# Optimization experiments

Measured on AMD Instinct MI355X. Metric: run time of the kernel, lower is better.

Reference implementation:

```python
import jax, jax.numpy as jnp
import numpy as np
from jax import lax

T, B, I, H = 32768, 1, 128, 512  # seq_len, batch(=1 due to squeeze(1)), input_dim, hidden_dim
HEAD = 25

def setup_inputs() -> dict:
    key = jax.random.key(0)
    ks = jax.random.split(key, 8)
    s = 1.0 / np.sqrt(H)  # pytorch LSTM init scale
    return {
        "x": jax.random.normal(ks[0], (T, B, I), dtype=jnp.float32),
        "W_ih": jax.random.uniform(ks[1], (4 * H, I), jnp.float32, -s, s),
        "W_hh": jax.random.uniform(ks[2], (4 * H, H), jnp.float32, -s, s),
        "b_ih": jax.random.uniform(ks[3], (4 * H,), jnp.float32, -s, s),
        "b_hh": jax.random.uniform(ks[4], (4 * H,), jnp.float32, -s, s),
        "W1": jax.random.uniform(ks[5], (HEAD, H), jnp.float32, -s, s),
        "b1": jax.random.uniform(ks[6], (HEAD,), jnp.float32, -s, s),
        "Wout": jax.random.uniform(ks[7], (1, HEAD), jnp.float32, -s, s),
    }

def reference(x, W_ih, W_hh, b_ih, b_hh, W1, b1, Wout):
    # Precompute input projections for all timesteps (one big GEMM): [T, B, 4H]
    xg = jnp.einsum('tbi,gi->tbg', x, W_ih) + (b_ih + b_hh)

    def step(carry, xg_t):
        h, c = carry  # [B, H] each
        gates = xg_t + h @ W_hh.T  # [B, 4H]
        i_g, f_g, g_g, o_g = jnp.split(gates, 4, axis=-1)  # pytorch gate order i,f,g,o
        i = jax.nn.sigmoid(i_g)
        f = jax.nn.sigmoid(f_g)
        g = jnp.tanh(g_g)
        o = jax.nn.sigmoid(o_g)
        c = f * c + i * g
        h = o * jnp.tanh(c)
        return (h, c), h

    h0 = jnp.zeros((B, H), x.dtype)
    _, hs = lax.scan(step, (h0, h0), xg)  # hs: [T, B, H]

    hid = hs[:, 0, :]  # h_1.squeeze(1) -> [T, H]
    # forward applies c1 then out (c2 is defined but unused in the original)
    out = (hid @ W1.T + b1) @ Wout.T  # [T, 1]
    return out
```

## Files before the change

kernel.cpp:

```cpp
#include <hip/hip_runtime.h>
#include <math.h>


#define T_SEQ 32768
#define HID   512
#define INP   128
#define NWG   32
#define NTH   512
#define HSL   16
#define KW    64
#define KX    16

typedef unsigned long long u64;

__device__ __forceinline__ float fast_sigmoid(float x) {
    return 1.0f / (1.0f + __expf(-x));
}
__device__ __forceinline__ float fast_tanh(float x) {
    float a = fabsf(x);
    float e = __expf(-2.0f * a);
    float r = (1.0f - e) / (1.0f + e);
    return copysignf(r, x);
}

__global__ void __launch_bounds__(NTH, 2) lstm_persist(
    const float* __restrict__ x,
    const float* __restrict__ W_ih,
    const float* __restrict__ W_hh,
    const float* __restrict__ b_ih,
    const float* __restrict__ b_hh,
    const float* __restrict__ W1,
    const float* __restrict__ Wout,
    u64* __restrict__ hbuf,
    float* __restrict__ out)
{
    const int w   = blockIdx.x;
    const int tid = threadIdx.x;
    const int rl  = tid >> 3;
    const int j   = tid & 7;
    const int grow = (rl >> 4) * HID + w * HSL + (rl & 15);

    __shared__ float h_lds[HID];
    __shared__ float gate_lds[64];

    float wr[KW];
#pragma unroll
    for (int kk = 0; kk < 16; ++kk) {
        const int p = (kk + 2 * j) & 15;
        const float4 wv = *(const float4*)&W_hh[grow * HID + j * KW + 4 * p];
        wr[4 * kk + 0] = wv.x; wr[4 * kk + 1] = wv.y;
        wr[4 * kk + 2] = wv.z; wr[4 * kk + 3] = wv.w;
    }
    float wi[KX];
#pragma unroll
    for (int k = 0; k < KX; k += 4) {
        const float4 wv = *(const float4*)&W_ih[grow * INP + j * KX + k];
        wi[k] = wv.x; wi[k + 1] = wv.y; wi[k + 2] = wv.z; wi[k + 3] = wv.w;
    }
    float brow = b_ih[grow] + b_hh[grow];
    float weff = 0.0f;
    if (tid < HSL) {
        const int col = w * HSL + tid;
        for (int p = 0; p < 25; ++p) weff += Wout[p] * W1[p * HID + col];
    }
#pragma unroll
    for (int k = 0; k < KW; ++k) asm volatile("" : "+v"(wr[k]));
#pragma unroll
    for (int k = 0; k < KX; ++k) asm volatile("" : "+v"(wi[k]));
    asm volatile("" : "+v"(brow));
    asm volatile("" : "+v"(weff));

    float c = 0.0f;
    float xa[KX];
#pragma unroll
    for (int k = 0; k < KX; ++k) xa[k] = x[j * KX + k];

    for (unsigned int t = 0; t < T_SEQ; ++t) {
        if (tid < 64) {
            const u64* P = hbuf + (t & 1) * HID;
            u64 pr[8];
            bool ok = false;
            do {
                if (!ok) {
                    ok = true;
#pragma unroll
                    for (int i = 0; i < 8; ++i) {
                        pr[i] = __hip_atomic_load(&P[tid + 64 * i],
                                                  __ATOMIC_RELAXED,
                                                  __HIP_MEMORY_SCOPE_AGENT);
                        ok = ok && ((unsigned int)(pr[i] >> 32) == t);
                    }
                }
            } while (__ballot(ok) != ~0ull);
#pragma unroll
            for (int i = 0; i < 8; ++i)
                h_lds[tid + 64 * i] = __uint_as_float((unsigned int)pr[i]);
        }
        __syncthreads();

        float a0 = 0.0f, a1 = 0.0f, a2 = 0.0f, a3 = 0.0f;
#pragma unroll
        for (int k = 0; k < KX; k += 4) {
            a0 += wi[k + 0] * xa[k + 0];
            a1 += wi[k + 1] * xa[k + 1];
            a2 += wi[k + 2] * xa[k + 2];
            a3 += wi[k + 3] * xa[k + 3];
        }
        const float4* hl4 = (const float4*)&h_lds[j * KW];
#pragma unroll
        for (int kk = 0; kk < 16; ++kk) {
            const int p = (kk + 2 * j) & 15;
            const float4 h4 = hl4[p];
            a0 += wr[4 * kk + 0] * h4.x;
            a1 += wr[4 * kk + 1] * h4.y;
            a2 += wr[4 * kk + 2] * h4.z;
            a3 += wr[4 * kk + 3] * h4.w;
        }
        const int tn = (t + 1 < T_SEQ) ? (int)(t + 1) : (int)t;
#pragma unroll
        for (int k = 0; k < KX; k += 4) {
            const float4 x4 = *(const float4*)&x[tn * INP + j * KX + k];
            xa[k + 0] = x4.x; xa[k + 1] = x4.y;
            xa[k + 2] = x4.z; xa[k + 3] = x4.w;
        }

        float acc = (a0 + a1) + (a2 + a3);
        acc += __shfl_xor(acc, 1);
        acc += __shfl_xor(acc, 2);
        acc += __shfl_xor(acc, 4);
        if (j == 0) gate_lds[rl] = acc + brow;
        __syncthreads();

        if (tid < HSL) {
            const float iv = fast_sigmoid(gate_lds[tid]);
            const float fv = fast_sigmoid(gate_lds[16 + tid]);
            const float gv = fast_tanh(gate_lds[32 + tid]);
            const float ov = fast_sigmoid(gate_lds[48 + tid]);
            c = fv * c + iv * gv;
            const float hv = ov * fast_tanh(c);
            const u64 pkt = ((u64)(t + 1) << 32) | (u64)__float_as_uint(hv);
            __hip_atomic_store(&hbuf[((t + 1) & 1) * HID + w * HSL + tid], pkt,
                               __ATOMIC_RELAXED, __HIP_MEMORY_SCOPE_AGENT);
            float pd = hv * weff;
            pd += __shfl_xor(pd, 1);
            pd += __shfl_xor(pd, 2);
            pd += __shfl_xor(pd, 4);
            pd += __shfl_xor(pd, 8);
            if (tid == 0) atomicAdd(&out[t], pd);
        }
    }
}

__global__ void init_out(const float* __restrict__ b1,
                         const float* __restrict__ Wout,
                         float* __restrict__ out)
{
    const int t = blockIdx.x * blockDim.x + threadIdx.x;
    float be = 0.0f;
    for (int p = 0; p < 25; ++p) be += b1[p] * Wout[p];
    if (t < T_SEQ) out[t] = be;
}

extern "C" void kernel_launch(void* const* d_in, const int* in_sizes, int n_in,
                              void* d_out, int out_size, void* d_ws, size_t ws_size,
                              hipStream_t stream)
{
    const float* x    = (const float*)d_in[0];
    const float* W_ih = (const float*)d_in[1];
    const float* W_hh = (const float*)d_in[2];
    const float* b_ih = (const float*)d_in[3];
    const float* b_hh = (const float*)d_in[4];
    const float* W1   = (const float*)d_in[5];
    const float* b1   = (const float*)d_in[6];
    const float* Wout = (const float*)d_in[7];
    float* out = (float*)d_out;

    u64* hbuf = (u64*)d_ws;

    hipMemsetAsync(d_ws, 0, 2 * HID * sizeof(u64), stream);
    init_out<<<(T_SEQ + 255) / 256, 256, 0, stream>>>(b1, Wout, out);
    lstm_persist<<<NWG, NTH, 0, stream>>>(x, W_ih, W_hh, b_ih, b_hh, W1, Wout,
                                          hbuf, out);
}
```

Measured before the change: 68.23 ms.

## Dedicate a polling wave and cut the per-step barrier and gate LDS round trip

Warp 0 of each block becomes a high-priority poller that copies the grid-exchanged hidden state into a double-buffered LDS array. The eight compute warps each own two hidden units and gather the four gate sums with wave shuffles instead of a second __syncthreads and a gate LDS array. The output head moves into block 0, which reduces the full hidden vector from the previous step and writes out[t-1] directly. This removes the init_out kernel and the global atomicAdd, and takes the output work off the recurrence critical path. The cost is one extra loop iteration and an extra wave per block, which changes the register and occupancy budget.

```diff
diff --git a/kernel.cpp b/kernel.cpp
--- a/kernel.cpp
+++ b/kernel.cpp
@@ -6,7 +6,7 @@
 #define HID   512
 #define INP   128
 #define NWG   32
-#define NTH   512
+#define NTH   576
 #define HSL   16
 #define KW    64
 #define KX    16
@@ -23,142 +23,186 @@
     return copysignf(r, x);
 }
 
-__global__ void __launch_bounds__(NTH, 2) lstm_persist(
+__global__ void __launch_bounds__(NTH, 1) lstm_persist(
     const float* __restrict__ x,
     const float* __restrict__ W_ih,
     const float* __restrict__ W_hh,
     const float* __restrict__ b_ih,
     const float* __restrict__ b_hh,
     const float* __restrict__ W1,
+    const float* __restrict__ b1,
     const float* __restrict__ Wout,
     u64* __restrict__ hbuf,
     float* __restrict__ out)
 {
     const int w   = blockIdx.x;
     const int tid = threadIdx.x;
-    const int rl  = tid >> 3;
-    const int j   = tid & 7;
-    const int grow = (rl >> 4) * HID + w * HSL + (rl & 15);
-
-    __shared__ float h_lds[HID];
-    __shared__ float gate_lds[64];
-
-    float wr[KW];
-#pragma unroll
-    for (int kk = 0; kk < 16; ++kk) {
-        const int p = (kk + 2 * j) & 15;
-        const float4 wv = *(const float4*)&W_hh[grow * HID + j * KW + 4 * p];
-        wr[4 * kk + 0] = wv.x; wr[4 * kk + 1] = wv.y;
-        wr[4 * kk + 2] = wv.z; wr[4 * kk + 3] = wv.w;
-    }
-    float wi[KX];
-#pragma unroll
-    for (int k = 0; k < KX; k += 4) {
-        const float4 wv = *(const float4*)&W_ih[grow * INP + j * KX + k];
-        wi[k] = wv.x; wi[k + 1] = wv.y; wi[k + 2] = wv.z; wi[k + 3] = wv.w;
-    }
-    float brow = b_ih[grow] + b_hh[grow];
-    float weff = 0.0f;
-    if (tid < HSL) {
-        const int col = w * HSL + tid;
-        for (int p = 0; p < 25; ++p) weff += Wout[p] * W1[p * HID + col];
+    const int wv  = (tid >> 6) - 1;
+    const int l   = tid & 63;
+    const int rw  = l >> 3;
+    const int j   = l & 7;
+    const int g   = rw >> 1;
+    const int b   = rw & 1;
+
+    const bool is_poll = (wv < 0);
+    const bool is_comp = (wv >= 0);
+    const bool is_out  = (w == 0 && wv == 0);
+
+    __shared__ float h_lds[2][HID];
+
+    int grow = 0;
+    float wr[KW], wi[KX];
+    float brow = 0.0f;
+#pragma unroll
+    for (int k = 0; k < KW; ++k) wr[k] = 0.0f;
+#pragma unroll
+    for (int k = 0; k < KX; ++k) wi[k] = 0.0f;
+    if (is_comp) {
+        grow = g * HID + w * HSL + 2 * wv + b;
+#pragma unroll
+        for (int kk = 0; kk < 16; ++kk) {
+            const int p = (kk + 2 * j) & 15;
+            const float4 v4 = *(const float4*)&W_hh[grow * HID + j * KW + 4 * p];
+            wr[4 * kk + 0] = v4.x; wr[4 * kk + 1] = v4.y;
+            wr[4 * kk + 2] = v4.z; wr[4 * kk + 3] = v4.w;
+        }
+#pragma unroll
+        for (int k = 0; k < KX; k += 4) {
+            const float4 v4 = *(const float4*)&W_ih[grow * INP + j * KX + k];
+            wi[k] = v4.x; wi[k + 1] = v4.y; wi[k + 2] = v4.z; wi[k + 3] = v4.w;
+        }
+        brow = b_ih[grow] + b_hh[grow];
+    }
+    float weff_o[8];
+    float be = 0.0f;
+#pragma unroll
+    for (int i = 0; i < 8; ++i) weff_o[i] = 0.0f;
+    if (is_out) {
+#pragma unroll
+        for (int i = 0; i < 8; ++i) {
+            float s = 0.0f;
+            for (int p = 0; p < 25; ++p) s += Wout[p] * W1[p * HID + l + 64 * i];
+            weff_o[i] = s;
+        }
+        for (int p = 0; p < 25; ++p) be += b1[p] * Wout[p];
     }
 #pragma unroll
     for (int k = 0; k < KW; ++k) asm volatile("" : "+v"(wr[k]));
 #pragma unroll
     for (int k = 0; k < KX; ++k) asm volatile("" : "+v"(wi[k]));
+#pragma unroll
+    for (int i = 0; i < 8; ++i) asm volatile("" : "+v"(weff_o[i]));
     asm volatile("" : "+v"(brow));
-    asm volatile("" : "+v"(weff));
+    asm volatile("" : "+v"(be));
+
+    if (is_poll) __builtin_amdgcn_s_setprio(3);
 
     float c = 0.0f;
     float xa[KX];
 #pragma unroll
-    for (int k = 0; k < KX; ++k) xa[k] = x[j * KX + k];
-
-    for (unsigned int t = 0; t < T_SEQ; ++t) {
-        if (tid < 64) {
+    for (int k = 0; k < KX; ++k) xa[k] = 0.0f;
+    if (is_comp) {
+#pragma unroll
+        for (int k = 0; k < KX; ++k) xa[k] = x[j * KX + k];
+    }
+
+    for (unsigned int t = 0; t <= T_SEQ; ++t) {
+        if (is_poll) {
             const u64* P = hbuf + (t & 1) * HID;
-            u64 pr[8];
-            bool ok = false;
-            do {
-                if (!ok) {
-                    ok = true;
+            bool mine = false;
+            while (true) {
+                if (!mine) {
+                    u64 pr[8];
+                    bool ok = true;
 #pragma unroll
                     for (int i = 0; i < 8; ++i) {
-                        pr[i] = __hip_atomic_load(&P[tid + 64 * i],
+                        pr[i] = __hip_atomic_load(&P[l + 64 * i],
                                                   __ATOMIC_RELAXED,
                                                   __HIP_MEMORY_SCOPE_AGENT);
                         ok = ok && ((unsigned int)(pr[i] >> 32) == t);
                     }
+                    if (ok) {
+#pragma unroll
+                        for (int i = 0; i < 8; ++i)
+                            h_lds[t & 1][l + 64 * i] =
+                                __uint_as_float((unsigned int)pr[i]);
+                        mine = true;
+                    }
                 }
-            } while (__ballot(ok) != ~0ull);
+                if (__ballot(mine) == ~0ull) break;
+            }
+        }
+        __syncthreads();
+
+        float hv = 0.0f;
+        if (is_comp && t < T_SEQ) {
+            float a0 = 0.0f, a1 = 0.0f, a2 = 0.0f, a3 = 0.0f;
+#pragma unroll
+            for (int k = 0; k < KX; k += 4) {
+                a0 += wi[k + 0] * xa[k + 0];
+                a1 += wi[k + 1] * xa[k + 1];
+                a2 += wi[k + 2] * xa[k + 2];
+                a3 += wi[k + 3] * xa[k + 3];
+            }
+            const float4* hl4 = (const float4*)&h_lds[t & 1][j * KW];
+#pragma unroll
+            for (int kk = 0; kk < 16; ++kk) {
+                const int p = (kk + 2 * j) & 15;
+                const float4 h4 = hl4[p];
+                a0 += wr[4 * kk + 0] * h4.x;
+                a1 += wr[4 * kk + 1] * h4.y;
+                a2 += wr[4 * kk + 2] * h4.z;
+                a3 += wr[4 * kk + 3] * h4.w;
+            }
+            const int tn = (t + 1 < T_SEQ) ? (int)(t + 1) : (T_SEQ - 1);
+#pragma unroll
+            for (int k = 0; k < KX; k += 4) {
+                const float4 x4 = *(const float4*)&x[tn * INP + j * KX + k];
+                xa[k + 0] = x4.x; xa[k + 1] = x4.y;
+                xa[k + 2] = x4.z; xa[k + 3] = x4.w;
+            }
+            float acc = (a0 + a1) + (a2 + a3);
+            acc += __shfl_xor(acc, 1);
+            acc += __shfl_xor(acc, 2);
+            acc += __shfl_xor(acc, 4);
+            acc += brow;
+            const float ig = acc;
+            const float fg = __shfl(acc, l + 16);
+            const float gg = __shfl(acc, l + 32);
+            const float og = __shfl(acc, l + 48);
+            const float iv = fast_sigmoid(ig);
+            const float fv = fast_sigmoid(fg);
+            const float gv = fast_tanh(gg);
+            const float ov = fast_sigmoid(og);
+            c = fv * c + iv * gv;
+            hv = ov * fast_tanh(c);
+        }
+
+        float pd = 0.0f;
+        if (is_out && t >= 1) {
 #pragma unroll
             for (int i = 0; i < 8; ++i)
-                h_lds[tid + 64 * i] = __uint_as_float((unsigned int)pr[i]);
-        }
-        __syncthreads();
-
-        float a0 = 0.0f, a1 = 0.0f, a2 = 0.0f, a3 = 0.0f;
-#pragma unroll
-        for (int k = 0; k < KX; k += 4) {
-            a0 += wi[k + 0] * xa[k + 0];
-            a1 += wi[k + 1] * xa[k + 1];
-            a2 += wi[k + 2] * xa[k + 2];
-            a3 += wi[k + 3] * xa[k + 3];
-        }
-        const float4* hl4 = (const float4*)&h_lds[j * KW];
-#pragma unroll
-        for (int kk = 0; kk < 16; ++kk) {
-            const int p = (kk + 2 * j) & 15;
-            const float4 h4 = hl4[p];
-            a0 += wr[4 * kk + 0] * h4.x;
-            a1 += wr[4 * kk + 1] * h4.y;
-            a2 += wr[4 * kk + 2] * h4.z;
-            a3 += wr[4 * kk + 3] * h4.w;
-        }
-        const int tn = (t + 1 < T_SEQ) ? (int)(t + 1) : (int)t;
-#pragma unroll
-        for (int k = 0; k < KX; k += 4) {
-            const float4 x4 = *(const float4*)&x[tn * INP + j * KX + k];
-            xa[k + 0] = x4.x; xa[k + 1] = x4.y;
-            xa[k + 2] = x4.z; xa[k + 3] = x4.w;
-        }
-
-        float acc = (a0 + a1) + (a2 + a3);
-        acc += __shfl_xor(acc, 1);
-        acc += __shfl_xor(acc, 2);
-        acc += __shfl_xor(acc, 4);
-        if (j == 0) gate_lds[rl] = acc + brow;
-        __syncthreads();
-
-        if (tid < HSL) {
-            const float iv = fast_sigmoid(gate_lds[tid]);
-            const float fv = fast_sigmoid(gate_lds[16 + tid]);
-            const float gv = fast_tanh(gate_lds[32 + tid]);
-            const float ov = fast_sigmoid(gate_lds[48 + tid]);
-            c = fv * c + iv * gv;
-            const float hv = ov * fast_tanh(c);
+                pd += h_lds[t & 1][l + 64 * i] * weff_o[i];
+        }
+        asm volatile("" ::: "memory");
+
+        if (is_comp && t < T_SEQ && (j == 0) && (g == 0)) {
+            const int e = w * HSL + 2 * wv + b;
             const u64 pkt = ((u64)(t + 1) << 32) | (u64)__float_as_uint(hv);
-            __hip_atomic_store(&hbuf[((t + 1) & 1) * HID + w * HSL + tid], pkt,
+            __hip_atomic_store(&hbuf[((t + 1) & 1) * HID + e], pkt,
                                __ATOMIC_RELAXED, __HIP_MEMORY_SCOPE_AGENT);
-            float pd = hv * weff;
+        }
+
+        if (is_out && t >= 1) {
             pd += __shfl_xor(pd, 1);
             pd += __shfl_xor(pd, 2);
             pd += __shfl_xor(pd, 4);
             pd += __shfl_xor(pd, 8);
-            if (tid == 0) atomicAdd(&out[t], pd);
-        }
-    }
-}
-
-__global__ void init_out(const float* __restrict__ b1,
-                         const float* __restrict__ Wout,
-                         float* __restrict__ out)
-{
-    const int t = blockIdx.x * blockDim.x + threadIdx.x;
-    float be = 0.0f;
-    for (int p = 0; p < 25; ++p) be += b1[p] * Wout[p];
-    if (t < T_SEQ) out[t] = be;
+            pd += __shfl_xor(pd, 16);
+            pd += __shfl_xor(pd, 32);
+            if (l == 0) out[t - 1] = pd + be;
+        }
+    }
 }
 
 extern "C" void kernel_launch(void* const* d_in, const int* in_sizes, int n_in,
@@ -178,7 +222,6 @@
     u64* hbuf = (u64*)d_ws;
 
     hipMemsetAsync(d_ws, 0, 2 * HID * sizeof(u64), stream);
-    init_out<<<(T_SEQ + 255) / 256, 256, 0, stream>>>(b1, Wout, out);
-    lstm_persist<<<NWG, NTH, 0, stream>>>(x, W_ih, W_hh, b_ih, b_hh, W1, Wout,
-                                          hbuf, out);
-}
+    lstm_persist<<<NWG, NTH, 0, stream>>>(x, W_ih, W_hh, b_ih, b_hh, W1, b1,
+                                          Wout, hbuf, out);
+}
```

Result: slower. 123.4 ms (+80.8%).
